# Kernel tuning notes

Hardware: AMD Instinct MI355X
Metric: run time of the kernel (lower is better)

The kernel has to match this reference:

```python
import jax, jax.numpy as jnp
import numpy as np

MAX_DELAY = 128
INPUT = 64
HIDDEN = 128
HALF = HIDDEN // 2
OUT = 64
B = 32
T = 128
OUT_LEN = 64


def setup_inputs() -> dict:
    key = jax.random.key(0)
    ks = jax.random.split(key, 10)
    w = lambda k, sh: (jax.random.normal(k, sh, jnp.float32) * 0.05)
    return {
        "x": jax.random.normal(ks[0], (B, T, INPUT), jnp.float32),
        "lengths": jax.random.randint(ks[1], (B,), 0, T, jnp.int32),
        "out_lengths": OUT_LEN,
        "Wm": w(ks[2], (INPUT + HIDDEN, HIDDEN)), "bm": jnp.zeros((HIDDEN,), jnp.float32),
        "W1": w(ks[3], (HIDDEN, HALF)), "b1": jnp.zeros((HALF,), jnp.float32),
        "W2": w(ks[4], (HALF, 2 * HIDDEN)), "b2": jnp.zeros((2 * HIDDEN,), jnp.float32),
        "Wo": w(ks[5], (HIDDEN, OUT)), "bo": jnp.zeros((OUT,), jnp.float32),
    }


def reference(x, lengths, out_lengths, Wm, bm, W1, b1, W2, b2, Wo, bo):
    # index_tensor: (1, 1, max_delay) in [0, 1)
    index = (jnp.arange(MAX_DELAY, dtype=x.dtype) / MAX_DELAY)[None, None, :]

    def tau_gen(msg):  # msg: (B, H)
        h = jax.nn.relu(msg @ W1 + b1)
        tg = jax.nn.sigmoid(h @ W2 + b2)  # (B, 2H)
        return tg[:, :HIDDEN], tg[:, HIDDEN:]

    def update_buffer(buffer, msg, tau, mem_i):
        # shift left, zero-pad at the end
        new_buf = jnp.pad(buffer[:, :, 1:], ((0, 0), (0, 0), (0, 1)))
        iw = mem_i[..., None] * (1.0 - jnp.abs(tau[..., None] - index)) ** 2  # (B,H,D)
        return (1.0 - iw) * new_buf + iw * msg[..., None]

    masks = (jnp.arange(T) < lengths[:, None]).astype(x.dtype)  # (B, T)

    def enc_step(buffer, inp):
        x_t, mask = inp  # (B, I), (B,)
        m = mask[:, None]  # (B, 1)
        msg = m * jnp.tanh(jnp.concatenate([x_t, buffer[:, :, 0]], axis=-1) @ Wm + bm)
        tau, mem_i = tau_gen(msg)
        new_buf = update_buffer(buffer, msg, tau, mem_i)
        buffer = jnp.where(m[..., None] > 0, new_buf, buffer)
        return buffer, None

    buffer0 = jnp.zeros((B, HIDDEN, MAX_DELAY), x.dtype)
    buffer, _ = jax.lax.scan(enc_step, buffer0, (x.transpose(1, 0, 2), masks.T))

    x0 = jnp.zeros((B, INPUT), x.dtype)

    def dec_step(buffer, _):
        msg = jnp.tanh(jnp.concatenate([x0, buffer[:, :, 0]], axis=-1) @ Wm + bm)
        tau, mem_i = tau_gen(msg)
        buffer = update_buffer(buffer, msg, tau, mem_i)
        return buffer, msg @ Wo + bo

    _, outs = jax.lax.scan(dec_step, buffer, None, length=out_lengths)
    return outs.transpose(1, 0, 2)  # (B, out_lengths, OUT)
```

## Files before the change

kernel.cpp:

```cpp
#include <hip/hip_runtime.h>
#include <math.h>

typedef __attribute__((ext_vector_type(2))) float f32x2;

#define MAX_DELAY 128
#define INPUT 64
#define HIDDEN 128
#define HALF 64
#define OUT 64
#define BATCH 32
#define T 128
#define OUT_LEN 64
#define NTHR 512

static __device__ __forceinline__ f32x2 splat2(float v) { f32x2 r; r.x = v; r.y = v; return r; }

template <int CTRL>
static __device__ __forceinline__ float dpp_movf(float v) {
    return __int_as_float(__builtin_amdgcn_update_dpp(
        0, __float_as_int(v), CTRL, 0xF, 0xF, true));
}
#define DPP_XOR1 0xB1
#define DPP_XOR2 0x4E
#define DPP_ROT1 0x39
#define DPP_MIR8 0x141

__global__ __launch_bounds__(NTHR, 2)
void delayrnn_kernel(
    const float* __restrict__ x,
    const int*   __restrict__ lengths,
    const float* __restrict__ Wm,
    const float* __restrict__ bm,
    const float* __restrict__ W1,
    const float* __restrict__ b1,
    const float* __restrict__ W2,
    const float* __restrict__ b2,
    const float* __restrict__ Wo,
    const float* __restrict__ bo,
    float* __restrict__ out)
{
    const int b   = blockIdx.x;
    const int tid = threadIdx.x;
    const int len = lengths[b];
    const int total = len + OUT_LEN;

    const int h  = tid >> 2, q  = tid & 3;
    const int qq = q & 1,    qh = q >> 1;
    const int k1 = tid >> 3, r1 = tid & 7;
    const int co = tid >> 3, ro = tid & 7;

    f32x2 wm2[24];
#pragma unroll
    for (int j = 0; j < 24; ++j) {
        wm2[j].x = Wm[(q * 48 + 2 * j)     * HIDDEN + h];
        wm2[j].y = Wm[(q * 48 + 2 * j + 1) * HIDDEN + h];
    }
    f32x2 w12[8];
#pragma unroll
    for (int j = 0; j < 8; ++j) {
        w12[j].x = W1[(r1 * 16 + 2 * j)     * HALF + k1];
        w12[j].y = W1[(r1 * 16 + 2 * j + 1) * HALF + k1];
    }
    const int c2 = h + 128 * qh;
    f32x2 w22[16];
#pragma unroll
    for (int j = 0; j < 16; ++j) {
        w22[j].x = W2[(qq * 32 + 2 * j)     * (2 * HIDDEN) + c2];
        w22[j].y = W2[(qq * 32 + 2 * j + 1) * (2 * HIDDEN) + c2];
    }
    f32x2 wo2[8];
#pragma unroll
    for (int j = 0; j < 8; ++j) {
        wo2[j].x = Wo[(ro * 16 + 2 * j)     * OUT + co];
        wo2[j].y = Wo[(ro * 16 + 2 * j + 1) * OUT + co];
    }
    const float bm_r = bm[h];
    const float b1_r = b1[k1];
    const float b2_r = b2[c2];
    const float bo_r = bo[co];

    float buf[32];
#pragma unroll
    for (int d = 0; d < 32; ++d) buf[d] = 0.f;

    __shared__ float s_x[T * INPUT];
    __shared__ float s_v[INPUT + HIDDEN];
    __shared__ float s_msg[HIDDEN];
    __shared__ float s_h1[HALF];

    for (int idx = tid; idx < T * INPUT; idx += NTHR)
        s_x[idx] = x[b * T * INPUT + idx];
    if (tid < INPUT) s_v[tid] = (0 < len) ? x[b * T * INPUT + tid] : 0.f;
    if (tid >= INPUT && tid < INPUT + HIDDEN) s_v[tid] = 0.f;
    __syncthreads();

    const float ivb = (float)q * 0.25f;

    for (int i = 0; i < total; ++i) {
        const f32x2* v2 = (const f32x2*)(s_v + q * 48);
        f32x2 a0 = splat2(0.f), a1 = splat2(0.f), a2 = splat2(0.f), a3 = splat2(0.f);
#pragma unroll
        for (int j = 0; j < 24; j += 4) {
            a0 += wm2[j] * v2[j];         a1 += wm2[j + 1] * v2[j + 1];
            a2 += wm2[j + 2] * v2[j + 2]; a3 += wm2[j + 3] * v2[j + 3];
        }
        f32x2 aa = (a0 + a1) + (a2 + a3);
        float p = aa.x + aa.y;
        p += dpp_movf<DPP_XOR1>(p);
        p += dpp_movf<DPP_XOR2>(p);
        const float z  = p + bm_r;
        const float e2 = __expf(2.f * z);
        const float msg = 1.f - 2.f * __builtin_amdgcn_rcpf(e2 + 1.f);
        if (q == 0) s_msg[h] = msg;
        __syncthreads();

        const f32x2* m2 = (const f32x2*)(s_msg + r1 * 16);
        f32x2 c0 = splat2(0.f), c1 = splat2(0.f);
#pragma unroll
        for (int j = 0; j < 8; j += 2) { c0 += w12[j] * m2[j]; c1 += w12[j + 1] * m2[j + 1]; }
        f32x2 cc = c0 + c1;
        float p1 = cc.x + cc.y;
        p1 += dpp_movf<DPP_XOR1>(p1);
        p1 += dpp_movf<DPP_XOR2>(p1);
        p1 += dpp_movf<DPP_MIR8>(p1);
        if (r1 == 0) s_h1[k1] = fmaxf(p1 + b1_r, 0.f);
        __syncthreads();

        const f32x2* h2 = (const f32x2*)(s_h1 + qq * 32);
        f32x2 t0 = splat2(0.f), t1 = splat2(0.f);
#pragma unroll
        for (int j = 0; j < 16; j += 2) { t0 += w22[j] * h2[j]; t1 += w22[j + 1] * h2[j + 1]; }
        f32x2 tt = t0 + t1;
        float pt = tt.x + tt.y;
        pt += dpp_movf<DPP_XOR1>(pt);
        const float own = __builtin_amdgcn_rcpf(1.f + __expf(-(pt + b2_r)));
        const float oth = dpp_movf<DPP_XOR2>(own);
        const float tau_r = qh ? oth : own;
        const float mem_r = qh ? own : oth;

        {
            float tail_in = dpp_movf<DPP_ROT1>(buf[0]);
            if (q == 3) tail_in = 0.f;
            const float taup = tau_r - ivb;
            const f32x2 tau2 = splat2(taup);
            const f32x2 mem2 = splat2(mem_r);
            const f32x2 m2m  = splat2(-2.f * mem_r);
            const f32x2 msg2 = splat2(msg);
#pragma unroll
            for (int mp = 0; mp < 16; ++mp) {
                const int d = 2 * mp;
                f32x2 nb;
                nb.x = buf[d + 1];
                nb.y = (mp < 15) ? buf[d + 2] : tail_in;
                f32x2 t;
                t.x = tau2.x - (float)d       * (1.f / MAX_DELAY);
                t.y = tau2.y - (float)(d + 1) * (1.f / MAX_DELAY);
                f32x2 a  = __builtin_elementwise_max(t, -t);
                f32x2 f1 = a * mem2 + m2m;
                f32x2 iw = a * f1 + mem2;
                f32x2 dd = msg2 - nb;
                f32x2 nv = iw * dd + nb;
                buf[d] = nv.x; buf[d + 1] = nv.y;
            }
        }
        if (q == 0) s_v[INPUT + h] = buf[0];

        if (i >= len) {
            const f32x2* mo2 = (const f32x2*)(s_msg + ro * 16);
            f32x2 o0 = splat2(0.f), o1 = splat2(0.f);
#pragma unroll
            for (int j = 0; j < 8; j += 2) { o0 += wo2[j] * mo2[j]; o1 += wo2[j + 1] * mo2[j + 1]; }
            f32x2 oo = o0 + o1;
            float po = oo.x + oo.y;
            po += dpp_movf<DPP_XOR1>(po);
            po += dpp_movf<DPP_XOR2>(po);
            po += dpp_movf<DPP_MIR8>(po);
            if (ro == 0) out[(b * OUT_LEN + (i - len)) * OUT + co] = po + bo_r;
        }

        if (tid < INPUT) {
            const int nx = i + 1;
            s_v[tid] = (nx < len) ? s_x[nx * INPUT + tid] : 0.f;
        }
        __syncthreads();
    }
}

extern "C" void kernel_launch(void* const* d_in, const int* in_sizes, int n_in,
                              void* d_out, int out_size, void* d_ws, size_t ws_size,
                              hipStream_t stream) {
    const float* x       = (const float*)d_in[0];
    const int*   lengths = (const int*)  d_in[1];
    const float* Wm = (const float*)d_in[3];
    const float* bm = (const float*)d_in[4];
    const float* W1 = (const float*)d_in[5];
    const float* b1 = (const float*)d_in[6];
    const float* W2 = (const float*)d_in[7];
    const float* b2 = (const float*)d_in[8];
    const float* Wo = (const float*)d_in[9];
    const float* bo = (const float*)d_in[10];
    float* out = (float*)d_out;

    delayrnn_kernel<<<BATCH, NTHR, 0, stream>>>(
        x, lengths, Wm, bm, W1, b1, W2, b2, Wo, bo, out);
}
```

Baseline: 323.2 us.

## Defer buffer update to next step and compute head element eagerly

```diff
diff --git a/kernel.cpp b/kernel.cpp
--- a/kernel.cpp
+++ b/kernel.cpp
@@ -2,6 +2,7 @@
 #include <math.h>
 
 typedef __attribute__((ext_vector_type(2))) float f32x2;
+typedef __attribute__((ext_vector_type(4))) float f32x4;
 
 #define MAX_DELAY 128
 #define INPUT 64
@@ -14,6 +15,7 @@
 #define NTHR 512
 
 static __device__ __forceinline__ f32x2 splat2(float v) { f32x2 r; r.x = v; r.y = v; return r; }
+static __device__ __forceinline__ f32x4 splat4(float v) { f32x4 r; r.x = v; r.y = v; r.z = v; r.w = v; return r; }
 
 template <int CTRL>
 static __device__ __forceinline__ float dpp_movf(float v) {
@@ -48,139 +50,160 @@
     const int qq = q & 1,    qh = q >> 1;
     const int k1 = tid >> 3, r1 = tid & 7;
     const int co = tid >> 3, ro = tid & 7;
-
-    f32x2 wm2[24];
-#pragma unroll
-    for (int j = 0; j < 24; ++j) {
-        wm2[j].x = Wm[(q * 48 + 2 * j)     * HIDDEN + h];
-        wm2[j].y = Wm[(q * 48 + 2 * j + 1) * HIDDEN + h];
-    }
-    f32x2 w12[8];
+    const int c2 = h + 128 * qh;
+
+    f32x4 wm4[12];
+#pragma unroll
+    for (int j = 0; j < 12; ++j) {
+        wm4[j].x = Wm[(q * 48 + 4 * j    ) * HIDDEN + h];
+        wm4[j].y = Wm[(q * 48 + 4 * j + 1) * HIDDEN + h];
+        wm4[j].z = Wm[(q * 48 + 4 * j + 2) * HIDDEN + h];
+        wm4[j].w = Wm[(q * 48 + 4 * j + 3) * HIDDEN + h];
+    }
+    f32x4 w14[4];
+#pragma unroll
+    for (int j = 0; j < 4; ++j) {
+        w14[j].x = W1[(r1 * 16 + 4 * j    ) * HALF + k1];
+        w14[j].y = W1[(r1 * 16 + 4 * j + 1) * HALF + k1];
+        w14[j].z = W1[(r1 * 16 + 4 * j + 2) * HALF + k1];
+        w14[j].w = W1[(r1 * 16 + 4 * j + 3) * HALF + k1];
+    }
+    f32x4 w24[8];
 #pragma unroll
     for (int j = 0; j < 8; ++j) {
-        w12[j].x = W1[(r1 * 16 + 2 * j)     * HALF + k1];
-        w12[j].y = W1[(r1 * 16 + 2 * j + 1) * HALF + k1];
-    }
-    const int c2 = h + 128 * qh;
-    f32x2 w22[16];
-#pragma unroll
-    for (int j = 0; j < 16; ++j) {
-        w22[j].x = W2[(qq * 32 + 2 * j)     * (2 * HIDDEN) + c2];
-        w22[j].y = W2[(qq * 32 + 2 * j + 1) * (2 * HIDDEN) + c2];
-    }
-    f32x2 wo2[8];
-#pragma unroll
-    for (int j = 0; j < 8; ++j) {
-        wo2[j].x = Wo[(ro * 16 + 2 * j)     * OUT + co];
-        wo2[j].y = Wo[(ro * 16 + 2 * j + 1) * OUT + co];
+        w24[j].x = W2[(qq * 32 + 4 * j    ) * (2 * HIDDEN) + c2];
+        w24[j].y = W2[(qq * 32 + 4 * j + 1) * (2 * HIDDEN) + c2];
+        w24[j].z = W2[(qq * 32 + 4 * j + 2) * (2 * HIDDEN) + c2];
+        w24[j].w = W2[(qq * 32 + 4 * j + 3) * (2 * HIDDEN) + c2];
+    }
+    f32x4 wo4[4];
+#pragma unroll
+    for (int m = 0; m < 4; ++m) {
+        wo4[m].x = Wo[(ro * 16 + 4 * m    ) * OUT + co];
+        wo4[m].y = Wo[(ro * 16 + 4 * m + 1) * OUT + co];
+        wo4[m].z = Wo[(ro * 16 + 4 * m + 2) * OUT + co];
+        wo4[m].w = Wo[(ro * 16 + 4 * m + 3) * OUT + co];
     }
     const float bm_r = bm[h];
     const float b1_r = b1[k1];
     const float b2_r = b2[c2];
     const float bo_r = bo[co];
 
-    float buf[32];
-#pragma unroll
-    for (int d = 0; d < 32; ++d) buf[d] = 0.f;
-
-    __shared__ float s_x[T * INPUT];
-    __shared__ float s_v[INPUT + HIDDEN];
-    __shared__ float s_msg[HIDDEN];
+    f32x2 buf2[16];
+#pragma unroll
+    for (int d = 0; d < 16; ++d) { buf2[d].x = 0.f; buf2[d].y = 0.f; }
+
+    __shared__ f32x4 s_x4[T * INPUT / 4];
+    __shared__ f32x4 s_v4[48];
+    __shared__ f32x4 s_msg4[48];
     __shared__ float s_h1[HALF];
 
-    for (int idx = tid; idx < T * INPUT; idx += NTHR)
-        s_x[idx] = x[b * T * INPUT + idx];
-    if (tid < INPUT) s_v[tid] = (0 < len) ? x[b * T * INPUT + tid] : 0.f;
-    if (tid >= INPUT && tid < INPUT + HIDDEN) s_v[tid] = 0.f;
+    {
+        const f32x4* xg4 = (const f32x4*)x;
+        for (int idx = tid; idx < T * INPUT / 4; idx += NTHR)
+            s_x4[idx] = xg4[b * (T * INPUT / 4) + idx];
+        if (tid < 16) s_v4[tid] = (0 < len) ? xg4[b * (T * INPUT / 4) + tid] : splat4(0.f);
+        if (tid >= 16 && tid < 48) s_v4[tid] = splat4(0.f);
+    }
     __syncthreads();
 
     const float ivb = (float)q * 0.25f;
+    float msg_p = 0.f, tau_p = 0.f, mem_p = 0.f;
 
     for (int i = 0; i < total; ++i) {
-        const f32x2* v2 = (const f32x2*)(s_v + q * 48);
-        f32x2 a0 = splat2(0.f), a1 = splat2(0.f), a2 = splat2(0.f), a3 = splat2(0.f);
-#pragma unroll
-        for (int j = 0; j < 24; j += 4) {
-            a0 += wm2[j] * v2[j];         a1 += wm2[j + 1] * v2[j + 1];
-            a2 += wm2[j + 2] * v2[j + 2]; a3 += wm2[j + 3] * v2[j + 3];
-        }
-        f32x2 aa = (a0 + a1) + (a2 + a3);
-        float p = aa.x + aa.y;
+        const f32x4* v4 = s_v4 + q * 12;
+        f32x4 a0 = splat4(0.f), a1 = splat4(0.f), a2 = splat4(0.f), a3 = splat4(0.f);
+#pragma unroll
+        for (int j = 0; j < 12; j += 4) {
+            a0 += wm4[j]     * v4[j];
+            a1 += wm4[j + 1] * v4[j + 1];
+            a2 += wm4[j + 2] * v4[j + 2];
+            a3 += wm4[j + 3] * v4[j + 3];
+        }
+
+        {
+            float tail_in = dpp_movf<DPP_ROT1>(buf2[0].x);
+            if (q == 3) tail_in = 0.f;
+            const float taup = tau_p - ivb;
+            f32x2 t2; t2.x = taup; t2.y = taup - (1.f / MAX_DELAY);
+            const f32x2 st2  = splat2(-2.f / MAX_DELAY);
+            const f32x2 mem2 = splat2(mem_p);
+            const f32x2 m2m  = splat2(-2.f * mem_p);
+            const f32x2 msg2 = splat2(msg_p);
+#pragma unroll
+            for (int d = 0; d < 16; ++d) {
+                f32x2 nb;
+                nb.x = buf2[d].y;
+                nb.y = (d < 15) ? buf2[d + 1].x : tail_in;
+                f32x2 a  = __builtin_elementwise_max(t2, -t2);
+                f32x2 f1 = a * mem2 + m2m;
+                f32x2 iw = a * f1 + mem2;
+                f32x2 dd = msg2 - nb;
+                buf2[d] = iw * dd + nb;
+                t2 = t2 + st2;
+            }
+        }
+
+        f32x4 s4 = (a0 + a1) + (a2 + a3);
+        float p = (s4.x + s4.z) + (s4.y + s4.w);
         p += dpp_movf<DPP_XOR1>(p);
         p += dpp_movf<DPP_XOR2>(p);
         const float z  = p + bm_r;
         const float e2 = __expf(2.f * z);
         const float msg = 1.f - 2.f * __builtin_amdgcn_rcpf(e2 + 1.f);
-        if (q == 0) s_msg[h] = msg;
+        if (q == 0) ((float*)s_msg4)[h + ((h >> 4) << 3)] = msg;
+        msg_p = msg;
         __syncthreads();
 
-        const f32x2* m2 = (const f32x2*)(s_msg + r1 * 16);
-        f32x2 c0 = splat2(0.f), c1 = splat2(0.f);
-#pragma unroll
-        for (int j = 0; j < 8; j += 2) { c0 += w12[j] * m2[j]; c1 += w12[j + 1] * m2[j + 1]; }
-        f32x2 cc = c0 + c1;
-        float p1 = cc.x + cc.y;
-        p1 += dpp_movf<DPP_XOR1>(p1);
-        p1 += dpp_movf<DPP_XOR2>(p1);
-        p1 += dpp_movf<DPP_MIR8>(p1);
-        if (r1 == 0) s_h1[k1] = fmaxf(p1 + b1_r, 0.f);
-        __syncthreads();
-
-        const f32x2* h2 = (const f32x2*)(s_h1 + qq * 32);
-        f32x2 t0 = splat2(0.f), t1 = splat2(0.f);
-#pragma unroll
-        for (int j = 0; j < 16; j += 2) { t0 += w22[j] * h2[j]; t1 += w22[j + 1] * h2[j + 1]; }
-        f32x2 tt = t0 + t1;
-        float pt = tt.x + tt.y;
-        pt += dpp_movf<DPP_XOR1>(pt);
-        const float own = __builtin_amdgcn_rcpf(1.f + __expf(-(pt + b2_r)));
-        const float oth = dpp_movf<DPP_XOR2>(own);
-        const float tau_r = qh ? oth : own;
-        const float mem_r = qh ? own : oth;
-
         {
-            float tail_in = dpp_movf<DPP_ROT1>(buf[0]);
-            if (q == 3) tail_in = 0.f;
-            const float taup = tau_r - ivb;
-            const f32x2 tau2 = splat2(taup);
-            const f32x2 mem2 = splat2(mem_r);
-            const f32x2 m2m  = splat2(-2.f * mem_r);
-            const f32x2 msg2 = splat2(msg);
-#pragma unroll
-            for (int mp = 0; mp < 16; ++mp) {
-                const int d = 2 * mp;
-                f32x2 nb;
-                nb.x = buf[d + 1];
-                nb.y = (mp < 15) ? buf[d + 2] : tail_in;
-                f32x2 t;
-                t.x = tau2.x - (float)d       * (1.f / MAX_DELAY);
-                t.y = tau2.y - (float)(d + 1) * (1.f / MAX_DELAY);
-                f32x2 a  = __builtin_elementwise_max(t, -t);
-                f32x2 f1 = a * mem2 + m2m;
-                f32x2 iw = a * f1 + mem2;
-                f32x2 dd = msg2 - nb;
-                f32x2 nv = iw * dd + nb;
-                buf[d] = nv.x; buf[d + 1] = nv.y;
-            }
-        }
-        if (q == 0) s_v[INPUT + h] = buf[0];
+            const f32x4* m4 = (const f32x4*)((const float*)s_msg4 + r1 * 24);
+            f32x4 cA = w14[0] * m4[0] + w14[2] * m4[2];
+            f32x4 cB = w14[1] * m4[1] + w14[3] * m4[3];
+            f32x4 cc = cA + cB;
+            float p1 = (cc.x + cc.z) + (cc.y + cc.w);
+            p1 += dpp_movf<DPP_XOR1>(p1);
+            p1 += dpp_movf<DPP_XOR2>(p1);
+            p1 += dpp_movf<DPP_MIR8>(p1);
+            if (r1 == 0) s_h1[k1] = fmaxf(p1 + b1_r, 0.f);
+        }
+
+        if (tid < 16) {
+            const int nx = i + 1;
+            f32x4 nv = splat4(0.f);
+            if (nx < len) nv = s_x4[nx * 16 + tid];
+            s_v4[tid] = nv;
+        }
 
         if (i >= len) {
-            const f32x2* mo2 = (const f32x2*)(s_msg + ro * 16);
-            f32x2 o0 = splat2(0.f), o1 = splat2(0.f);
-#pragma unroll
-            for (int j = 0; j < 8; j += 2) { o0 += wo2[j] * mo2[j]; o1 += wo2[j + 1] * mo2[j + 1]; }
-            f32x2 oo = o0 + o1;
-            float po = oo.x + oo.y;
+            const f32x4* mo4 = s_msg4 + ro * 6;
+            f32x4 oA = wo4[0] * mo4[0] + wo4[2] * mo4[2];
+            f32x4 oB = wo4[1] * mo4[1] + wo4[3] * mo4[3];
+            f32x4 oo = oA + oB;
+            float po = (oo.x + oo.z) + (oo.y + oo.w);
             po += dpp_movf<DPP_XOR1>(po);
             po += dpp_movf<DPP_XOR2>(po);
             po += dpp_movf<DPP_MIR8>(po);
             if (ro == 0) out[(b * OUT_LEN + (i - len)) * OUT + co] = po + bo_r;
         }
-
-        if (tid < INPUT) {
-            const int nx = i + 1;
-            s_v[tid] = (nx < len) ? s_x[nx * INPUT + tid] : 0.f;
+        __syncthreads();
+
+        {
+            const f32x4* hh4 = (const f32x4*)(s_h1 + (qq << 5));
+            f32x4 tA = w24[0] * hh4[0] + w24[2] * hh4[2] + w24[4] * hh4[4] + w24[6] * hh4[6];
+            f32x4 tB = w24[1] * hh4[1] + w24[3] * hh4[3] + w24[5] * hh4[5] + w24[7] * hh4[7];
+            f32x4 tt = tA + tB;
+            float pt = (tt.x + tt.z) + (tt.y + tt.w);
+            pt += dpp_movf<DPP_XOR1>(pt);
+            const float own = __builtin_amdgcn_rcpf(1.f + __expf(-(pt + b2_r)));
+            const float oth = dpp_movf<DPP_XOR2>(own);
+            const float tau_r = qh ? oth : own;
+            const float mem_r = qh ? own : oth;
+            tau_p = tau_r; mem_p = mem_r;
+
+            const float nb0 = buf2[0].y;
+            const float iw0 = tau_r * (tau_r * mem_r - 2.f * mem_r) + mem_r;
+            const float head = iw0 * (msg_p - nb0) + nb0;
+            if (q == 0) ((float*)s_v4)[INPUT + h] = head;
         }
         __syncthreads();
     }
```

Result: faster. 314.3 us (-2.8%).
